# Kernel optimization log

Measured on AMD Instinct MI355X. Metric: run time of the kernel, lower is better.

The kernel has to match this reference:

```python
import jax, jax.numpy as jnp
import numpy as np

B, N, C = 8192, 4, 1024
H = 16
D = C // H              # head_dim = 64
P = 4                   # proj_dim (Linformer reduced length)
IDX_I, IDX_J = 1, 2     # Return_attn_way(use_cls=True, attn_selet_way=0)
SCALE = D ** -0.5


def setup_inputs() -> dict:
    key = jax.random.key(0)
    ks = jax.random.split(key, 6)
    std = 0.02
    x = jax.random.normal(ks[0], (B, N, C), dtype=jnp.float32)
    W_qkv = jax.random.normal(ks[1], (C, 3 * C), dtype=jnp.float32) * std   # qkv_bias=False
    W_proj = jax.random.normal(ks[2], (C, C), dtype=jnp.float32) * std
    b_proj = jnp.zeros((C,), dtype=jnp.float32)
    W_E = jax.random.normal(ks[3], (P, N), dtype=jnp.float32) * std         # torch Linear weight [out,in]
    W_F = jax.random.normal(ks[4], (P, N), dtype=jnp.float32) * std
    return {"x": x, "W_qkv": W_qkv, "W_proj": W_proj, "b_proj": b_proj,
            "W_E": W_E, "W_F": W_F}


def reference(x, W_qkv, W_proj, b_proj, W_E, W_F):
    b, n, c = x.shape
    # qkv projection -> [B,N,3,H,D] -> q,k,v each [B,H,N,D]
    qkv = (x @ W_qkv).reshape(b, n, 3, H, D)
    qkv = jnp.transpose(qkv, (2, 0, 3, 1, 4))
    q, k, v = qkv[0], qkv[1], qkv[2]
    q = q * SCALE  # q_norm/k_norm are Identity (qk_norm=False)

    # gathered single-token score: q[:,:,IDX_I,:] @ k[:,:,IDX_J,:].T -> [B,H,H]
    # (torch transpose(-2,-1) on the [B,H,D] slice swaps H and D)
    attn_sel = jnp.einsum('bhd,bgd->bhg', q[:, :, IDX_I, :], k[:, :, IDX_J, :])
    attn_sel_sig = jax.nn.sigmoid(attn_sel)

    # Linformer E/F projection along the sequence axis: [B,H,N,D] -> [B,H,P,D]
    k_low = jnp.einsum('bhnd,pn->bhpd', k, W_E)
    v_low = jnp.einsum('bhnd,pn->bhpd', v, W_F)

    # reduced softmax attention: [B,H,N,P]
    attn = jnp.einsum('bhnd,bhpd->bhnp', q, k_low)
    attn = jax.nn.softmax(attn, axis=-1)  # attn_drop is identity (p=0, eval)
    out = jnp.einsum('bhnp,bhpd->bhnd', attn, v_low)

    # merge heads and output projection
    out = jnp.transpose(out, (0, 2, 1, 3)).reshape(b, n, c)
    out = out @ W_proj.T + b_proj  # proj_drop identity
    return (out, attn_sel_sig)
```

## Files before the change

kernel.cpp:

```cpp
#include <hip/hip_runtime.h>
#include <hip/hip_bf16.h>

#define B_   8192
#define C_   1024
#define H_   16
#define M_   (B_ * 4)
#define K_   1024
#define N1_  3072

typedef __attribute__((ext_vector_type(8))) short short8;
typedef __attribute__((ext_vector_type(4))) float f32x4;
typedef __attribute__((ext_vector_type(8))) int   int8v;

__device__ __forceinline__ unsigned short f2bf(float f) {
  union { float f; unsigned u; } v; v.f = f;
  unsigned r = v.u + 0x7fffu + ((v.u >> 16) & 1u);
  return (unsigned short)(r >> 16);
}
__device__ __forceinline__ float bf2f(unsigned short u) {
  union { unsigned u; float f; } v; v.u = ((unsigned)u) << 16;
  return v.f;
}
__device__ __forceinline__ int pk_fp8(float a, float b, float c, float d) {
  int r = __builtin_amdgcn_cvt_pk_fp8_f32(a, b, 0, false);
  r = __builtin_amdgcn_cvt_pk_fp8_f32(c, d, r, true);
  return r;
}

__global__ __launch_bounds__(256) void cast_x_k(const float* __restrict__ x,
                                                unsigned char* __restrict__ x8,
                                                unsigned short* __restrict__ xsel) {
  const int row = blockIdx.x;
  const int tid = threadIdx.x;
  float4 v = ((const float4*)(x + (size_t)row * 1024))[tid];
  ((int*)(x8 + (size_t)row * 1024))[tid] = pk_fp8(v.x, v.y, v.z, v.w);
  const int n = row & 3;
  if (n == 1 || n == 2) {
    ushort4 o;
    o.x = f2bf(v.x); o.y = f2bf(v.y); o.z = f2bf(v.z); o.w = f2bf(v.w);
    ((ushort4*)(xsel + ((size_t)(n - 1) * 8192 + (row >> 2)) * 1024))[tid] = o;
  }
}

__global__ __launch_bounds__(256) void transpose_wqkv_k(const float* __restrict__ in,
                                                        unsigned short* __restrict__ outb,
                                                        unsigned char* __restrict__ out8) {
  __shared__ float t[32][33];
  int tx = threadIdx.x, ty = threadIdx.y;
  int j0 = blockIdx.x * 32, c0 = blockIdx.y * 32;
#pragma unroll
  for (int i = 0; i < 4; ++i)
    t[ty + i * 8][tx] = in[(size_t)(c0 + ty + i * 8) * N1_ + j0 + tx];
  __syncthreads();
#pragma unroll
  for (int i = 0; i < 4; ++i) {
    int j = j0 + ty + i * 8;
    float v = t[tx][ty + i * 8];
    if (j < 1024) v *= 0.125f;
    outb[(size_t)j * K_ + c0 + tx] = f2bf(v);
    out8[(size_t)j * K_ + c0 + tx] =
        (unsigned char)(__builtin_amdgcn_cvt_pk_fp8_f32(v * 32.f, v * 32.f, 0, false) & 0xff);
  }
}

__global__ __launch_bounds__(256) void cast_wproj_k(const float* __restrict__ in,
                                                    unsigned char* __restrict__ out) {
  int i = blockIdx.x * 256 + threadIdx.x;
  float4 v = ((const float4*)in)[i];
  ((int*)out)[i] = pk_fp8(v.x * 32.f, v.y * 32.f, v.z * 32.f, v.w * 32.f);
}

__global__ __launch_bounds__(256) void gemm_fixup(const unsigned short* __restrict__ A,
                                                  const unsigned short* __restrict__ B0,
                                                  unsigned short* __restrict__ Cbf) {
  __shared__ unsigned short lsA[128 * 32];
  __shared__ unsigned short lsB[128 * 32];
  const int K = 1024, Ncols = 1024;
  const int tid = threadIdx.x;
  const int wave = tid >> 6, lane = tid & 63;
  const int wm = (wave >> 1) * 64, wn = (wave & 1) * 64;
  const long tile_m = (long)blockIdx.y * 128, tile_n = (long)blockIdx.x * 128;
  const unsigned short* Bm = B0 + (tile_m >= 8192 ? (size_t)1024 * 1024 : 0);

  f32x4 acc[4][4] = {};
  const int ci0 = (wave * 2 + 0) * 64 + lane;
  const int ci1 = (wave * 2 + 1) * 64 + lane;
  const int r0 = ci0 >> 2, kc0 = (ci0 & 3) * 8;
  const int r1 = ci1 >> 2, kc1 = (ci1 & 3) * 8;
  const unsigned short* gA0 = A + (tile_m + r0) * K + kc0;
  const unsigned short* gA1 = A + (tile_m + r1) * K + kc1;
  const unsigned short* gB0 = Bm + (tile_n + r0) * K + kc0;
  const unsigned short* gB1 = Bm + (tile_n + r1) * K + kc1;
  unsigned short* dA0 = lsA + (wave * 2 + 0) * 512;
  unsigned short* dA1 = lsA + (wave * 2 + 1) * 512;
  unsigned short* dB0 = lsB + (wave * 2 + 0) * 512;
  unsigned short* dB1 = lsB + (wave * 2 + 1) * 512;
  const int r16 = lane & 15, q8 = (lane >> 4) * 8;

  for (int kt = 0; kt < K; kt += 32) {
    __builtin_amdgcn_global_load_lds((const __attribute__((address_space(1))) void*)(gA0 + kt),
                                     (__attribute__((address_space(3))) void*)dA0, 16, 0, 0);
    __builtin_amdgcn_global_load_lds((const __attribute__((address_space(1))) void*)(gA1 + kt),
                                     (__attribute__((address_space(3))) void*)dA1, 16, 0, 0);
    __builtin_amdgcn_global_load_lds((const __attribute__((address_space(1))) void*)(gB0 + kt),
                                     (__attribute__((address_space(3))) void*)dB0, 16, 0, 0);
    __builtin_amdgcn_global_load_lds((const __attribute__((address_space(1))) void*)(gB1 + kt),
                                     (__attribute__((address_space(3))) void*)dB1, 16, 0, 0);
    __syncthreads();
    short8 afr[4], bfr[4];
#pragma unroll
    for (int mi = 0; mi < 4; ++mi)
      afr[mi] = *(const short8*)&lsA[(wm + mi * 16 + r16) * 32 + q8];
#pragma unroll
    for (int ni = 0; ni < 4; ++ni)
      bfr[ni] = *(const short8*)&lsB[(wn + ni * 16 + r16) * 32 + q8];
#pragma unroll
    for (int mi = 0; mi < 4; ++mi)
#pragma unroll
      for (int ni = 0; ni < 4; ++ni)
        acc[mi][ni] = __builtin_amdgcn_mfma_f32_16x16x32_bf16(afr[mi], bfr[ni], acc[mi][ni], 0, 0, 0);
    __syncthreads();
  }
  const int cl = lane & 15, rq = (lane >> 4) * 4;
#pragma unroll
  for (int mi = 0; mi < 4; ++mi)
#pragma unroll
    for (int ni = 0; ni < 4; ++ni) {
      long col = tile_n + wn + ni * 16 + cl;
#pragma unroll
      for (int r = 0; r < 4; ++r) {
        long row = tile_m + wm + mi * 16 + rq + r;
        Cbf[(size_t)row * Ncols + col] = f2bf(acc[mi][ni][r]);
      }
    }
}

template <int OUTMODE>
__global__ __launch_bounds__(256) void gemm_mx(const unsigned char* __restrict__ A,
                                               const unsigned char* __restrict__ Bm,
                                               unsigned short* __restrict__ Cbf,
                                               float* __restrict__ Cf,
                                               const float* __restrict__ bias,
                                               int K, int Ncols, int sA, int sB) {
  __shared__ unsigned char lsA[16384];
  __shared__ unsigned char lsB[16384];
  const int tid = threadIdx.x;
  const int wave = tid >> 6, lane = tid & 63;
  const int wm = (wave >> 1) * 64, wn = (wave & 1) * 64;
  const long tile_m = (long)blockIdx.y * 128, tile_n = (long)blockIdx.x * 128;

  f32x4 acc[4][4] = {};

  size_t offA[4], offB[4];
#pragma unroll
  for (int j = 0; j < 4; ++j) {
    int ci = j * 256 + tid;
    int qg = ci >> 8, id = ci & 255;
    int r2 = (id >> 3) & 1, r3 = (id >> 4) & 1;
    int rr0 = ((id >> 1) & 1) ^ r2, rr1 = ((id >> 2) & 1) ^ r3;
    int row = rr0 | (rr1 << 1) | (r2 << 2) | (r3 << 3) | ((id >> 5) << 4);
    int half = (id & 1) ^ rr0;
    offA[j] = (size_t)(tile_m + row) * K + qg * 32 + half * 16;
    offB[j] = (size_t)(tile_n + row) * K + qg * 32 + half * 16;
  }

  const int hl = lane & 15, qg = lane >> 4;
  const int swz = (hl & 12) << 3;
  const int laneFragBase = qg * 4096 + ((hl * 32) ^ swz) + ((hl & 1) << 4);

  for (int kt = 0; kt < K; kt += 128) {
#pragma unroll
    for (int j = 0; j < 4; ++j) {
      __builtin_amdgcn_global_load_lds(
          (const __attribute__((address_space(1))) void*)(A + offA[j] + kt),
          (__attribute__((address_space(3))) void*)(lsA + (j * 256 + wave * 64) * 16), 16, 0, 0);
      __builtin_amdgcn_global_load_lds(
          (const __attribute__((address_space(1))) void*)(Bm + offB[j] + kt),
          (__attribute__((address_space(3))) void*)(lsB + (j * 256 + wave * 64) * 16), 16, 0, 0);
    }
    __syncthreads();

    int8v af[4], bfr[4];
#pragma unroll
    for (int mi = 0; mi < 4; ++mi) {
      int ad = (wm + mi * 16) * 32 + laneFragBase;
      int4 h0 = *(const int4*)(lsA + ad);
      int4 h1 = *(const int4*)(lsA + (ad ^ 16));
      af[mi] = int8v{h0.x, h0.y, h0.z, h0.w, h1.x, h1.y, h1.z, h1.w};
    }
#pragma unroll
    for (int ni = 0; ni < 4; ++ni) {
      int ad = (wn + ni * 16) * 32 + laneFragBase;
      int4 h0 = *(const int4*)(lsB + ad);
      int4 h1 = *(const int4*)(lsB + (ad ^ 16));
      bfr[ni] = int8v{h0.x, h0.y, h0.z, h0.w, h1.x, h1.y, h1.z, h1.w};
    }
#pragma unroll
    for (int mi = 0; mi < 4; ++mi)
#pragma unroll
      for (int ni = 0; ni < 4; ++ni)
        acc[mi][ni] = __builtin_amdgcn_mfma_scale_f32_16x16x128_f8f6f4(
            af[mi], bfr[ni], acc[mi][ni], 0, 0, 0, sA, 0, sB);
    __syncthreads();
  }

  const int cl = lane & 15, rq = (lane >> 4) * 4;
#pragma unroll
  for (int mi = 0; mi < 4; ++mi)
#pragma unroll
    for (int ni = 0; ni < 4; ++ni) {
      long col = tile_n + wn + ni * 16 + cl;
      float bv = (OUTMODE == 1) ? bias[col] : 0.f;
#pragma unroll
      for (int r = 0; r < 4; ++r) {
        long row = tile_m + wm + mi * 16 + rq + r;
        if (OUTMODE == 0)
          Cbf[(size_t)row * Ncols + col] = f2bf(acc[mi][ni][r]);
        else
          Cf[(size_t)row * Ncols + col] = acc[mi][ni][r] + bv;
      }
    }
}

__global__ __launch_bounds__(256) void attn_mfma_k(const unsigned short* __restrict__ qkv,
                                                   const unsigned short* __restrict__ q1,
                                                   const unsigned short* __restrict__ k2,
                                                   const float* __restrict__ WE,
                                                   const float* __restrict__ WF,
                                                   unsigned char* __restrict__ hmid8,
                                                   float* __restrict__ attn_sel) {
  __shared__ float As[4][16 * 17 + 2];
  const int tid = threadIdx.x;
  const int wave = tid >> 6, lane = tid & 63;
  const int b = blockIdx.x * 4 + wave;
  const size_t qb = (size_t)b * 4 * N1_;
  const int hl = lane & 15, qg = lane >> 4;

  f32x4 accS[4][4] = {};
  f32x4 accSel = {};
#pragma unroll
  for (int ch = 0; ch < 2; ++ch) {
    const int off = ch * 32 + qg * 8;
    short8 qf[4], kf[4];
#pragma unroll
    for (int n = 0; n < 4; ++n)
      qf[n] = *(const short8*)(qkv + qb + (size_t)n * N1_ + 0 + hl * 64 + off);
#pragma unroll
    for (int m = 0; m < 4; ++m)
      kf[m] = *(const short8*)(qkv + qb + (size_t)m * N1_ + 1024 + hl * 64 + off);
#pragma unroll
    for (int n = 0; n < 4; ++n)
#pragma unroll
      for (int m = 0; m < 4; ++m)
        accS[n][m] = __builtin_amdgcn_mfma_f32_16x16x32_bf16(qf[n], kf[m], accS[n][m], 0, 0, 0);
    short8 qs = *(const short8*)(q1 + (size_t)b * 1024 + hl * 64 + off);
    short8 ks = *(const short8*)(k2 + (size_t)b * 1024 + hl * 64 + off);
    accSel = __builtin_amdgcn_mfma_f32_16x16x32_bf16(qs, ks, accSel, 0, 0, 0);
  }

#pragma unroll
  for (int r = 0; r < 4; ++r)
    attn_sel[(size_t)b * 256 + (qg * 4 + r) * 16 + hl] = 1.f / (1.f + __expf(-accSel[r]));

  if ((hl >> 2) == qg) {
    const int h = hl, rr = h & 3;
    float Sm[4][4];
#pragma unroll
    for (int n = 0; n < 4; ++n)
#pragma unroll
      for (int m = 0; m < 4; ++m) Sm[n][m] = accS[n][m][rr];
#pragma unroll
    for (int n = 0; n < 4; ++n) {
      float lg[4];
#pragma unroll
      for (int p = 0; p < 4; ++p)
        lg[p] = Sm[n][0] * WE[p * 4] + Sm[n][1] * WE[p * 4 + 1] +
                Sm[n][2] * WE[p * 4 + 2] + Sm[n][3] * WE[p * 4 + 3];
      float mx = fmaxf(fmaxf(lg[0], lg[1]), fmaxf(lg[2], lg[3]));
      float e0 = __expf(lg[0] - mx), e1 = __expf(lg[1] - mx);
      float e2 = __expf(lg[2] - mx), e3 = __expf(lg[3] - mx);
      float inv = 1.f / (e0 + e1 + e2 + e3);
      e0 *= inv; e1 *= inv; e2 *= inv; e3 *= inv;
#pragma unroll
      for (int m = 0; m < 4; ++m)
        As[wave][h * 17 + n * 4 + m] =
            e0 * WF[0 * 4 + m] + e1 * WF[1 * 4 + m] + e2 * WF[2 * 4 + m] + e3 * WF[3 * 4 + m];
    }
  }
  __syncthreads();

  {
    const int h = lane & 15, dg = lane >> 4;
    float Ap[4][4];
#pragma unroll
    for (int n = 0; n < 4; ++n)
#pragma unroll
      for (int m = 0; m < 4; ++m) Ap[n][m] = As[wave][h * 17 + n * 4 + m];

    float outv[4][16] = {};
#pragma unroll
    for (int m = 0; m < 4; ++m) {
      const unsigned short* vp = qkv + qb + (size_t)m * N1_ + 2048 + h * 64 + dg * 16;
      short8 v0 = *(const short8*)(vp);
      short8 v1 = *(const short8*)(vp + 8);
      float vf[16];
#pragma unroll
      for (int j = 0; j < 8; ++j) {
        vf[j] = bf2f((unsigned short)v0[j]);
        vf[8 + j] = bf2f((unsigned short)v1[j]);
      }
#pragma unroll
      for (int n = 0; n < 4; ++n)
#pragma unroll
        for (int d = 0; d < 16; ++d) outv[n][d] += Ap[n][m] * vf[d];
    }
#pragma unroll
    for (int n = 0; n < 4; ++n) {
      int w0 = pk_fp8(outv[n][0] * 32.f, outv[n][1] * 32.f, outv[n][2] * 32.f, outv[n][3] * 32.f);
      int w1 = pk_fp8(outv[n][4] * 32.f, outv[n][5] * 32.f, outv[n][6] * 32.f, outv[n][7] * 32.f);
      int w2 = pk_fp8(outv[n][8] * 32.f, outv[n][9] * 32.f, outv[n][10] * 32.f, outv[n][11] * 32.f);
      int w3 = pk_fp8(outv[n][12] * 32.f, outv[n][13] * 32.f, outv[n][14] * 32.f, outv[n][15] * 32.f);
      *(int4*)(hmid8 + ((size_t)b * 4 + n) * 1024 + h * 64 + dg * 16) = make_int4(w0, w1, w2, w3);
    }
  }
}

extern "C" void kernel_launch(void* const* d_in, const int* in_sizes, int n_in,
                              void* d_out, int out_size, void* d_ws, size_t ws_size,
                              hipStream_t stream) {
  (void)in_sizes; (void)n_in; (void)out_size; (void)ws_size;
  const float* x      = (const float*)d_in[0];
  const float* W_qkv  = (const float*)d_in[1];
  const float* W_proj = (const float*)d_in[2];
  const float* b_proj = (const float*)d_in[3];
  const float* W_E    = (const float*)d_in[4];
  const float* W_F    = (const float*)d_in[5];

  float* out0 = (float*)d_out;
  float* out1 = out0 + (size_t)M_ * C_;

  char* ws = (char*)d_ws;
  unsigned short* xsel   = (unsigned short*)(ws);
  unsigned short* wqkvTb = (unsigned short*)(ws + 33554432);
  unsigned short* qkv_bf = (unsigned short*)(ws);
  unsigned char*  x8     = (unsigned char*)(ws + 201326592);
  unsigned char*  hmid8  = x8;
  unsigned char*  wqkvT8 = (unsigned char*)(ws + 234881024);
  unsigned char*  wproj8 = (unsigned char*)(ws + 238026752);
  unsigned short* q1k2   = (unsigned short*)(ws + 239075328);

  cast_x_k<<<32768, 256, 0, stream>>>(x, x8, xsel);
  transpose_wqkv_k<<<dim3(96, 32), dim3(32, 8), 0, stream>>>(W_qkv, wqkvTb, wqkvT8);
  cast_wproj_k<<<1024, 256, 0, stream>>>(W_proj, wproj8);

  gemm_fixup<<<dim3(8, 128), 256, 0, stream>>>(xsel, wqkvTb, q1k2);

  gemm_mx<0><<<dim3(24, 256), 256, 0, stream>>>(x8, wqkvT8, qkv_bf, nullptr, nullptr,
                                                1024, 3072, 127, 122);

  attn_mfma_k<<<B_ / 4, 256, 0, stream>>>(qkv_bf, q1k2, q1k2 + (size_t)8192 * 1024,
                                          W_E, W_F, hmid8, out1);

  gemm_mx<1><<<dim3(8, 256), 256, 0, stream>>>(hmid8, wproj8, nullptr, out0, b_proj,
                                               1024, 1024, 122, 122);
}
```

Before: 576.8 us.

## Enlarge FP8 GEMM tiles to 256x256 with double-buffered LDS pipeline

```diff
diff --git a/kernel.cpp b/kernel.cpp
--- a/kernel.cpp
+++ b/kernel.cpp
@@ -136,77 +136,112 @@
 }
 
 template <int OUTMODE>
-__global__ __launch_bounds__(256) void gemm_mx(const unsigned char* __restrict__ A,
+__global__ __launch_bounds__(512) void gemm_mx(const unsigned char* __restrict__ A,
                                                const unsigned char* __restrict__ Bm,
                                                unsigned short* __restrict__ Cbf,
                                                float* __restrict__ Cf,
                                                const float* __restrict__ bias,
                                                int K, int Ncols, int sA, int sB) {
-  __shared__ unsigned char lsA[16384];
-  __shared__ unsigned char lsB[16384];
+  __shared__ unsigned char lds[131072];
+  unsigned char* lsA0 = lds;
+  unsigned char* lsB0 = lds + 32768;
+  unsigned char* lsA1 = lds + 65536;
+  unsigned char* lsB1 = lds + 98304;
+
   const int tid = threadIdx.x;
   const int wave = tid >> 6, lane = tid & 63;
-  const int wm = (wave >> 1) * 64, wn = (wave & 1) * 64;
-  const long tile_m = (long)blockIdx.y * 128, tile_n = (long)blockIdx.x * 128;
-
-  f32x4 acc[4][4] = {};
-
-  size_t offA[4], offB[4];
+  const int wm = (wave >> 2) * 128;
+  const int wn = (wave & 3) * 64;
+  const long tile_m = (long)blockIdx.y * 256, tile_n = (long)blockIdx.x * 256;
+
+  f32x4 acc[8][4] = {};
+
+  unsigned offA[4], offB[4];
 #pragma unroll
   for (int j = 0; j < 4; ++j) {
-    int ci = j * 256 + tid;
-    int qg = ci >> 8, id = ci & 255;
+    int ci = j * 512 + tid;
+    int blk = ci >> 10, idb = ci & 1023;
+    int qg = idb >> 8, id = idb & 255;
     int r2 = (id >> 3) & 1, r3 = (id >> 4) & 1;
     int rr0 = ((id >> 1) & 1) ^ r2, rr1 = ((id >> 2) & 1) ^ r3;
     int row = rr0 | (rr1 << 1) | (r2 << 2) | (r3 << 3) | ((id >> 5) << 4);
     int half = (id & 1) ^ rr0;
-    offA[j] = (size_t)(tile_m + row) * K + qg * 32 + half * 16;
-    offB[j] = (size_t)(tile_n + row) * K + qg * 32 + half * 16;
-  }
+    offA[j] = (unsigned)((tile_m + blk * 128 + row) * K + qg * 32 + half * 16);
+    offB[j] = (unsigned)((tile_n + blk * 128 + row) * K + qg * 32 + half * 16);
+  }
+
+  auto stage = [&](int kt, unsigned char* lA, unsigned char* lB) {
+#pragma unroll
+    for (int j = 0; j < 4; ++j)
+      __builtin_amdgcn_global_load_lds(
+          (const __attribute__((address_space(1))) void*)(A + offA[j] + kt),
+          (__attribute__((address_space(3))) void*)(lA + j * 8192 + wave * 1024), 16, 0, 0);
+#pragma unroll
+    for (int j = 0; j < 4; ++j)
+      __builtin_amdgcn_global_load_lds(
+          (const __attribute__((address_space(1))) void*)(Bm + offB[j] + kt),
+          (__attribute__((address_space(3))) void*)(lB + j * 8192 + wave * 1024), 16, 0, 0);
+  };
 
   const int hl = lane & 15, qg = lane >> 4;
   const int swz = (hl & 12) << 3;
   const int laneFragBase = qg * 4096 + ((hl * 32) ^ swz) + ((hl & 1) << 4);
-
-  for (int kt = 0; kt < K; kt += 128) {
-#pragma unroll
-    for (int j = 0; j < 4; ++j) {
-      __builtin_amdgcn_global_load_lds(
-          (const __attribute__((address_space(1))) void*)(A + offA[j] + kt),
-          (__attribute__((address_space(3))) void*)(lsA + (j * 256 + wave * 64) * 16), 16, 0, 0);
-      __builtin_amdgcn_global_load_lds(
-          (const __attribute__((address_space(1))) void*)(Bm + offB[j] + kt),
-          (__attribute__((address_space(3))) void*)(lsB + (j * 256 + wave * 64) * 16), 16, 0, 0);
-    }
-    __syncthreads();
-
-    int8v af[4], bfr[4];
-#pragma unroll
-    for (int mi = 0; mi < 4; ++mi) {
-      int ad = (wm + mi * 16) * 32 + laneFragBase;
-      int4 h0 = *(const int4*)(lsA + ad);
-      int4 h1 = *(const int4*)(lsA + (ad ^ 16));
-      af[mi] = int8v{h0.x, h0.y, h0.z, h0.w, h1.x, h1.y, h1.z, h1.w};
-    }
+  const int Abase = (wm >> 7) * 16384 + laneFragBase;
+  const int Bbase = (wn >> 7) * 16384 + (wn & 64) * 32 + laneFragBase;
+
+  const int NT = K >> 7;
+  stage(0, lsA0, lsB0);
+  stage(128, lsA1, lsB1);
+  asm volatile("s_waitcnt vmcnt(8)" ::: "memory");
+  __builtin_amdgcn_s_barrier();
+
+  for (int t = 0; t < NT; ++t) {
+    unsigned char* lA = (t & 1) ? lsA1 : lsA0;
+    unsigned char* lB = (t & 1) ? lsB1 : lsB0;
+
+    int8v bfr[4];
 #pragma unroll
     for (int ni = 0; ni < 4; ++ni) {
-      int ad = (wn + ni * 16) * 32 + laneFragBase;
-      int4 h0 = *(const int4*)(lsB + ad);
-      int4 h1 = *(const int4*)(lsB + (ad ^ 16));
+      int ad = Bbase + ni * 512;
+      int4 h0 = *(const int4*)(lB + ad);
+      int4 h1 = *(const int4*)(lB + (ad ^ 16));
       bfr[ni] = int8v{h0.x, h0.y, h0.z, h0.w, h1.x, h1.y, h1.z, h1.w};
     }
 #pragma unroll
-    for (int mi = 0; mi < 4; ++mi)
-#pragma unroll
-      for (int ni = 0; ni < 4; ++ni)
-        acc[mi][ni] = __builtin_amdgcn_mfma_scale_f32_16x16x128_f8f6f4(
-            af[mi], bfr[ni], acc[mi][ni], 0, 0, 0, sA, 0, sB);
-    __syncthreads();
+    for (int p = 0; p < 4; ++p) {
+      int8v af[2];
+#pragma unroll
+      for (int mm = 0; mm < 2; ++mm) {
+        int ad = Abase + (p * 2 + mm) * 512;
+        int4 h0 = *(const int4*)(lA + ad);
+        int4 h1 = *(const int4*)(lA + (ad ^ 16));
+        af[mm] = int8v{h0.x, h0.y, h0.z, h0.w, h1.x, h1.y, h1.z, h1.w};
+      }
+      __builtin_amdgcn_s_barrier();
+      asm volatile("s_waitcnt lgkmcnt(0)" ::: "memory");
+      __builtin_amdgcn_s_setprio(1);
+#pragma unroll
+      for (int mm = 0; mm < 2; ++mm)
+#pragma unroll
+        for (int ni = 0; ni < 4; ++ni)
+          acc[p * 2 + mm][ni] = __builtin_amdgcn_mfma_scale_f32_16x16x128_f8f6f4(
+              af[mm], bfr[ni], acc[p * 2 + mm][ni], 0, 0, 0, sA, 0, sB);
+      __builtin_amdgcn_s_setprio(0);
+      __builtin_amdgcn_s_barrier();
+    }
+    if (t + 2 < NT) {
+      stage((t + 2) << 7, lA, lB);
+      asm volatile("s_waitcnt vmcnt(8)" ::: "memory");
+      __builtin_amdgcn_s_barrier();
+    } else if (t + 1 < NT) {
+      asm volatile("s_waitcnt vmcnt(0)" ::: "memory");
+      __builtin_amdgcn_s_barrier();
+    }
   }
 
   const int cl = lane & 15, rq = (lane >> 4) * 4;
 #pragma unroll
-  for (int mi = 0; mi < 4; ++mi)
+  for (int mi = 0; mi < 8; ++mi)
 #pragma unroll
     for (int ni = 0; ni < 4; ++ni) {
       long col = tile_n + wn + ni * 16 + cl;
@@ -355,12 +390,12 @@
 
   gemm_fixup<<<dim3(8, 128), 256, 0, stream>>>(xsel, wqkvTb, q1k2);
 
-  gemm_mx<0><<<dim3(24, 256), 256, 0, stream>>>(x8, wqkvT8, qkv_bf, nullptr, nullptr,
+  gemm_mx<0><<<dim3(12, 128), 512, 0, stream>>>(x8, wqkvT8, qkv_bf, nullptr, nullptr,
                                                 1024, 3072, 127, 122);
 
   attn_mfma_k<<<B_ / 4, 256, 0, stream>>>(qkv_bf, q1k2, q1k2 + (size_t)8192 * 1024,
                                           W_E, W_F, hmid8, out1);
 
-  gemm_mx<1><<<dim3(8, 256), 256, 0, stream>>>(hmid8, wproj8, nullptr, out0, b_proj,
+  gemm_mx<1><<<dim3(4, 128), 512, 0, stream>>>(hmid8, wproj8, nullptr, out0, b_proj,
                                                1024, 1024, 122, 122);
 }
```

Result: slower. 599.9 us (+4.0%).

## Load GEMM B fragments directly from global memory instead of staging in LDS

Applied to the files above, without the earlier changes.

```diff
diff --git a/kernel.cpp b/kernel.cpp
--- a/kernel.cpp
+++ b/kernel.cpp
@@ -74,7 +74,6 @@
                                                   const unsigned short* __restrict__ B0,
                                                   unsigned short* __restrict__ Cbf) {
   __shared__ unsigned short lsA[128 * 32];
-  __shared__ unsigned short lsB[128 * 32];
   const int K = 1024, Ncols = 1024;
   const int tid = threadIdx.x;
   const int wave = tid >> 6, lane = tid & 63;
@@ -89,31 +88,25 @@
   const int r1 = ci1 >> 2, kc1 = (ci1 & 3) * 8;
   const unsigned short* gA0 = A + (tile_m + r0) * K + kc0;
   const unsigned short* gA1 = A + (tile_m + r1) * K + kc1;
-  const unsigned short* gB0 = Bm + (tile_n + r0) * K + kc0;
-  const unsigned short* gB1 = Bm + (tile_n + r1) * K + kc1;
   unsigned short* dA0 = lsA + (wave * 2 + 0) * 512;
   unsigned short* dA1 = lsA + (wave * 2 + 1) * 512;
-  unsigned short* dB0 = lsB + (wave * 2 + 0) * 512;
-  unsigned short* dB1 = lsB + (wave * 2 + 1) * 512;
   const int r16 = lane & 15, q8 = (lane >> 4) * 8;
+  const unsigned short* gBf = Bm + (size_t)(tile_n + wn + r16) * K + q8;
 
   for (int kt = 0; kt < K; kt += 32) {
     __builtin_amdgcn_global_load_lds((const __attribute__((address_space(1))) void*)(gA0 + kt),
                                      (__attribute__((address_space(3))) void*)dA0, 16, 0, 0);
     __builtin_amdgcn_global_load_lds((const __attribute__((address_space(1))) void*)(gA1 + kt),
                                      (__attribute__((address_space(3))) void*)dA1, 16, 0, 0);
-    __builtin_amdgcn_global_load_lds((const __attribute__((address_space(1))) void*)(gB0 + kt),
-                                     (__attribute__((address_space(3))) void*)dB0, 16, 0, 0);
-    __builtin_amdgcn_global_load_lds((const __attribute__((address_space(1))) void*)(gB1 + kt),
-                                     (__attribute__((address_space(3))) void*)dB1, 16, 0, 0);
+    short8 bfr[4];
+#pragma unroll
+    for (int ni = 0; ni < 4; ++ni)
+      bfr[ni] = *(const short8*)(gBf + (size_t)ni * 16 * K + kt);
     __syncthreads();
-    short8 afr[4], bfr[4];
+    short8 afr[4];
 #pragma unroll
     for (int mi = 0; mi < 4; ++mi)
       afr[mi] = *(const short8*)&lsA[(wm + mi * 16 + r16) * 32 + q8];
-#pragma unroll
-    for (int ni = 0; ni < 4; ++ni)
-      bfr[ni] = *(const short8*)&lsB[(wn + ni * 16 + r16) * 32 + q8];
 #pragma unroll
     for (int mi = 0; mi < 4; ++mi)
 #pragma unroll
@@ -143,7 +136,6 @@
                                                const float* __restrict__ bias,
                                                int K, int Ncols, int sA, int sB) {
   __shared__ unsigned char lsA[16384];
-  __shared__ unsigned char lsB[16384];
   const int tid = threadIdx.x;
   const int wave = tid >> 6, lane = tid & 63;
   const int wm = (wave >> 1) * 64, wn = (wave & 1) * 64;
@@ -151,7 +143,7 @@
 
   f32x4 acc[4][4] = {};
 
-  size_t offA[4], offB[4];
+  size_t offA[4];
 #pragma unroll
   for (int j = 0; j < 4; ++j) {
     int ci = j * 256 + tid;
@@ -161,39 +153,37 @@
     int row = rr0 | (rr1 << 1) | (r2 << 2) | (r3 << 3) | ((id >> 5) << 4);
     int half = (id & 1) ^ rr0;
     offA[j] = (size_t)(tile_m + row) * K + qg * 32 + half * 16;
-    offB[j] = (size_t)(tile_n + row) * K + qg * 32 + half * 16;
   }
 
   const int hl = lane & 15, qg = lane >> 4;
   const int swz = (hl & 12) << 3;
   const int laneFragBase = qg * 4096 + ((hl * 32) ^ swz) + ((hl & 1) << 4);
+  const unsigned char* gBf = Bm + (size_t)(tile_n + wn + hl) * K + qg * 32;
 
   for (int kt = 0; kt < K; kt += 128) {
 #pragma unroll
-    for (int j = 0; j < 4; ++j) {
+    for (int j = 0; j < 4; ++j)
       __builtin_amdgcn_global_load_lds(
           (const __attribute__((address_space(1))) void*)(A + offA[j] + kt),
           (__attribute__((address_space(3))) void*)(lsA + (j * 256 + wave * 64) * 16), 16, 0, 0);
-      __builtin_amdgcn_global_load_lds(
-          (const __attribute__((address_space(1))) void*)(Bm + offB[j] + kt),
-          (__attribute__((address_space(3))) void*)(lsB + (j * 256 + wave * 64) * 16), 16, 0, 0);
+
+    int8v bfr[4];
+#pragma unroll
+    for (int ni = 0; ni < 4; ++ni) {
+      const unsigned char* bp = gBf + (size_t)ni * 16 * K + kt;
+      int4 h0 = *(const int4*)bp;
+      int4 h1 = *(const int4*)(bp + 16);
+      bfr[ni] = int8v{h0.x, h0.y, h0.z, h0.w, h1.x, h1.y, h1.z, h1.w};
     }
     __syncthreads();
 
-    int8v af[4], bfr[4];
+    int8v af[4];
 #pragma unroll
     for (int mi = 0; mi < 4; ++mi) {
       int ad = (wm + mi * 16) * 32 + laneFragBase;
       int4 h0 = *(const int4*)(lsA + ad);
       int4 h1 = *(const int4*)(lsA + (ad ^ 16));
       af[mi] = int8v{h0.x, h0.y, h0.z, h0.w, h1.x, h1.y, h1.z, h1.w};
-    }
-#pragma unroll
-    for (int ni = 0; ni < 4; ++ni) {
-      int ad = (wn + ni * 16) * 32 + laneFragBase;
-      int4 h0 = *(const int4*)(lsB + ad);
-      int4 h1 = *(const int4*)(lsB + (ad ^ 16));
-      bfr[ni] = int8v{h0.x, h0.y, h0.z, h0.w, h1.x, h1.y, h1.z, h1.w};
     }
 #pragma unroll
     for (int mi = 0; mi < 4; ++mi)
```

New measurement: 693.4 us. +20.2%, slower.
